# Kernel optimization log

Measured on AMD Instinct MI355X. Metric: run time of the kernel, lower is better.

## Reference

```python
import jax, jax.numpy as jnp
import numpy as np

B, T, D, O = 16, 1024, 1024, 10  # broadcast in original requires T == D

def setup_inputs() -> dict:
    key = jax.random.key(0)
    k1, k2, k3 = jax.random.split(key, 3)
    logits = jax.random.normal(k1, (B, T, D), dtype=jnp.float32)
    decision = jax.random.uniform(k2, (B, T, O), dtype=jnp.float32)  # unused by forward math
    W = jax.random.normal(k3, (O, D), dtype=jnp.float32) * 0.02  # attention.weight
    b = jnp.zeros((O,), dtype=jnp.float32)                       # attention.bias
    return {"logits": logits, "decision": decision, "W": W, "b": b}

def reference(logits, decision, W, b):
    outputdim = W.shape[0]
    # w_x = softmax(Linear(logits)/outputdim, dim=1)  -> softmax over time T
    scores = (jnp.einsum('btd,od->bto', logits, W) + b) / outputdim  # (B,T,O)
    w_x = jax.nn.softmax(scores, axis=1)
    # Original materializes h[b,i,o,t] = logits[b,t,i] * w_x[b,i,o] (needs T==D),
    # then flattens (o,t) and sums over dim 1 (i). Equivalent contraction:
    # out[b,o,t] = sum_i logits[b,t,i] * w_x[b,i,o]
    out = jnp.einsum('bti,bio->bot', logits, w_x)  # (B,O,T)
    return out.reshape(logits.shape[0], -1)        # (B, O*T)
```

## Files before the change

kernel.cpp:

```cpp
#include <hip/hip_runtime.h>

#define BB 16
#define TT 1024
#define DD 1024
#define OO 10

template <bool BIAS>
__global__ __launch_bounds__(256) void gemm10_kernel(
    const float* __restrict__ X,
    const float* __restrict__ Wt,
    const float* __restrict__ bias,
    float* __restrict__ Y,
    float scale, int perBatchW)
{
    __shared__ float sW[OO * DD];
    __shared__ float part[4][32][OO];

    const int b   = blockIdx.y;
    const int t0  = blockIdx.x * 32;
    const int tid = threadIdx.x;

    {
        const float4* src = (const float4*)(Wt + (size_t)(perBatchW ? b : 0) * (OO * DD));
        float4* dst = (float4*)sW;
#pragma unroll
        for (int c = 0; c < 10; ++c)
            dst[c * 256 + tid] = src[c * 256 + tid];
    }
    __syncthreads();

    const int w    = tid >> 6;
    const int lane = tid & 63;
    const int l    = lane & 7;
    const int g    = lane >> 3;
    const int dofs = w * 256 + l * 4;

    const float* xp[4];
#pragma unroll
    for (int j = 0; j < 4; ++j)
        xp[j] = X + ((size_t)b * TT + t0 + g + 8 * j) * DD + dofs;
    const float* sWl = sW + dofs;

    float acc[4][OO];
#pragma unroll
    for (int j = 0; j < 4; ++j)
#pragma unroll
        for (int o = 0; o < OO; ++o) acc[j][o] = 0.f;

    float4 x0[4], x1[4];
#pragma unroll
    for (int j = 0; j < 4; ++j) {
        x0[j] = *(const float4*)(xp[j]);
        x1[j] = *(const float4*)(xp[j] + 32);
    }

#pragma unroll 1
    for (int it = 0; it < 8; it += 2) {
        float4 c0[4];
#pragma unroll
        for (int j = 0; j < 4; ++j) c0[j] = x0[j];
        if (it < 6) {
#pragma unroll
            for (int j = 0; j < 4; ++j)
                x0[j] = *(const float4*)(xp[j] + (it + 2) * 32);
        }
        {
            const float* wp = sWl + it * 32;
#pragma unroll
            for (int o = 0; o < OO; ++o) {
                const float4 wv = *(const float4*)(wp + o * DD);
#pragma unroll
                for (int j = 0; j < 4; ++j)
                    acc[j][o] += c0[j].x * wv.x + c0[j].y * wv.y +
                                 c0[j].z * wv.z + c0[j].w * wv.w;
            }
        }
#pragma unroll
        for (int j = 0; j < 4; ++j) c0[j] = x1[j];
        if (it < 5) {
#pragma unroll
            for (int j = 0; j < 4; ++j)
                x1[j] = *(const float4*)(xp[j] + (it + 3) * 32);
        }
        {
            const float* wp = sWl + (it + 1) * 32;
#pragma unroll
            for (int o = 0; o < OO; ++o) {
                const float4 wv = *(const float4*)(wp + o * DD);
#pragma unroll
                for (int j = 0; j < 4; ++j)
                    acc[j][o] += c0[j].x * wv.x + c0[j].y * wv.y +
                                 c0[j].z * wv.z + c0[j].w * wv.w;
            }
        }
    }

#pragma unroll
    for (int j = 0; j < 4; ++j) {
#pragma unroll
        for (int o = 0; o < OO; ++o) {
            float v = acc[j][o];
            v += __shfl_down(v, 4, 8);
            v += __shfl_down(v, 2, 8);
            v += __shfl_down(v, 1, 8);
            if (l == 0) part[w][j * 8 + g][o] = v;
        }
    }
    __syncthreads();

    for (int idx = tid; idx < 32 * OO; idx += 256) {
        const int row = idx / OO;
        const int o   = idx % OO;
        float v = part[0][row][o] + part[1][row][o] +
                  part[2][row][o] + part[3][row][o];
        if (BIAS) v = (v + bias[o]) * scale;
        Y[((size_t)b * OO + o) * TT + (t0 + row)] = v;
    }
}

__global__ __launch_bounds__(256) void softmax_kernel(float* __restrict__ s)
{
    float* col = s + (size_t)blockIdx.x * TT;
    const int tid  = threadIdx.x;
    const int wave = tid >> 6;
    const int lane = tid & 63;

    float4 v = *(const float4*)(col + tid * 4);

    __shared__ float sm[4];
    __shared__ float ss[4];

    float m = fmaxf(fmaxf(v.x, v.y), fmaxf(v.z, v.w));
#pragma unroll
    for (int off = 32; off > 0; off >>= 1) m = fmaxf(m, __shfl_down(m, off, 64));
    if (lane == 0) sm[wave] = m;
    __syncthreads();
    m = fmaxf(fmaxf(sm[0], sm[1]), fmaxf(sm[2], sm[3]));

    float e0 = __expf(v.x - m), e1 = __expf(v.y - m);
    float e2 = __expf(v.z - m), e3 = __expf(v.w - m);
    float sum = e0 + e1 + e2 + e3;
#pragma unroll
    for (int off = 32; off > 0; off >>= 1) sum += __shfl_down(sum, off, 64);
    if (lane == 0) ss[wave] = sum;
    __syncthreads();
    const float inv = 1.0f / (ss[0] + ss[1] + ss[2] + ss[3]);

    *(float4*)(col + tid * 4) = make_float4(e0 * inv, e1 * inv, e2 * inv, e3 * inv);
}

extern "C" void kernel_launch(void* const* d_in, const int* in_sizes, int n_in,
                              void* d_out, int out_size, void* d_ws, size_t ws_size,
                              hipStream_t stream)
{
    const float* logits = (const float*)d_in[0];
    const float* W    = (const float*)d_in[2];
    const float* bias = (const float*)d_in[3];
    float* out    = (float*)d_out;
    float* scores = (float*)d_ws;

    dim3 grid(TT / 32, BB);
    gemm10_kernel<true><<<grid, 256, 0, stream>>>(logits, W, bias, scores,
                                                  1.0f / OO, 0);
    softmax_kernel<<<BB * OO, 256, 0, stream>>>(scores);
    gemm10_kernel<false><<<grid, 256, 0, stream>>>(logits, scores, nullptr, out,
                                                   1.0f, 1);
}
```

Baseline: 120.7 us.

## Stage X tiles through padded double-buffered shared memory for coalesced loads

```diff
diff --git a/kernel.cpp b/kernel.cpp
--- a/kernel.cpp
+++ b/kernel.cpp
@@ -13,8 +13,9 @@
     float* __restrict__ Y,
     float scale, int perBatchW)
 {
-    __shared__ float sW[OO * DD];
-    __shared__ float part[4][32][OO];
+    __shared__ float4 sW4[OO * 256];
+    __shared__ float4 sX[2][32 * 33];
+    __shared__ float  part[4][32][OO];
 
     const int b   = blockIdx.y;
     const int t0  = blockIdx.x * 32;
@@ -22,10 +23,23 @@
 
     {
         const float4* src = (const float4*)(Wt + (size_t)(perBatchW ? b : 0) * (OO * DD));
-        float4* dst = (float4*)sW;
 #pragma unroll
         for (int c = 0; c < 10; ++c)
-            dst[c * 256 + tid] = src[c * 256 + tid];
+            sW4[c * 256 + tid] = src[c * 256 + tid];
+    }
+
+    const int srow = tid >> 5;
+    const int scol = tid & 31;
+    const float4* Xb = (const float4*)(X + ((size_t)b * TT + t0) * DD);
+
+    {
+        float4 st[4];
+#pragma unroll
+        for (int k = 0; k < 4; ++k)
+            st[k] = Xb[(size_t)(srow + 8 * k) * 256 + scol];
+#pragma unroll
+        for (int k = 0; k < 4; ++k)
+            sX[0][(srow + 8 * k) * 33 + scol] = st[k];
     }
     __syncthreads();
 
@@ -33,13 +47,7 @@
     const int lane = tid & 63;
     const int l    = lane & 7;
     const int g    = lane >> 3;
-    const int dofs = w * 256 + l * 4;
-
-    const float* xp[4];
-#pragma unroll
-    for (int j = 0; j < 4; ++j)
-        xp[j] = X + ((size_t)b * TT + t0 + g + 8 * j) * DD + dofs;
-    const float* sWl = sW + dofs;
+    const int xoff = w * 8 + l;
 
     float acc[4][OO];
 #pragma unroll
@@ -47,52 +55,35 @@
 #pragma unroll
         for (int o = 0; o < OO; ++o) acc[j][o] = 0.f;
 
-    float4 x0[4], x1[4];
+#pragma unroll 1
+    for (int c = 0; c < 8; ++c) {
+        float4 st[4];
+        if (c < 7) {
 #pragma unroll
-    for (int j = 0; j < 4; ++j) {
-        x0[j] = *(const float4*)(xp[j]);
-        x1[j] = *(const float4*)(xp[j] + 32);
-    }
+            for (int k = 0; k < 4; ++k)
+                st[k] = Xb[(size_t)(srow + 8 * k) * 256 + (c + 1) * 32 + scol];
+        }
 
-#pragma unroll 1
-    for (int it = 0; it < 8; it += 2) {
-        float4 c0[4];
+        const float4* xb = sX[c & 1];
+        float4 xf[4];
 #pragma unroll
-        for (int j = 0; j < 4; ++j) c0[j] = x0[j];
-        if (it < 6) {
+        for (int j = 0; j < 4; ++j)
+            xf[j] = xb[(g + 8 * j) * 33 + xoff];
+#pragma unroll
+        for (int o = 0; o < OO; ++o) {
+            const float4 wv = sW4[o * 256 + c * 32 + xoff];
 #pragma unroll
             for (int j = 0; j < 4; ++j)
-                x0[j] = *(const float4*)(xp[j] + (it + 2) * 32);
+                acc[j][o] += xf[j].x * wv.x + xf[j].y * wv.y +
+                             xf[j].z * wv.z + xf[j].w * wv.w;
         }
-        {
-            const float* wp = sWl + it * 32;
+
+        if (c < 7) {
 #pragma unroll
-            for (int o = 0; o < OO; ++o) {
-                const float4 wv = *(const float4*)(wp + o * DD);
-#pragma unroll
-                for (int j = 0; j < 4; ++j)
-                    acc[j][o] += c0[j].x * wv.x + c0[j].y * wv.y +
-                                 c0[j].z * wv.z + c0[j].w * wv.w;
-            }
+            for (int k = 0; k < 4; ++k)
+                sX[(c + 1) & 1][(srow + 8 * k) * 33 + scol] = st[k];
         }
-#pragma unroll
-        for (int j = 0; j < 4; ++j) c0[j] = x1[j];
-        if (it < 5) {
-#pragma unroll
-            for (int j = 0; j < 4; ++j)
-                x1[j] = *(const float4*)(xp[j] + (it + 3) * 32);
-        }
-        {
-            const float* wp = sWl + (it + 1) * 32;
-#pragma unroll
-            for (int o = 0; o < OO; ++o) {
-                const float4 wv = *(const float4*)(wp + o * DD);
-#pragma unroll
-                for (int j = 0; j < 4; ++j)
-                    acc[j][o] += c0[j].x * wv.x + c0[j].y * wv.y +
-                                 c0[j].z * wv.z + c0[j].w * wv.w;
-            }
-        }
+        __syncthreads();
     }
 
 #pragma unroll
```

Result: slower. 144.4 us (+19.6%).

## Fuse score GEMM, softmax, and pooling GEMM into one kernel with per-batch barrier

Applied to the files above, without the earlier changes.

```diff
diff --git a/kernel.cpp b/kernel.cpp
--- a/kernel.cpp
+++ b/kernel.cpp
@@ -5,27 +5,27 @@
 #define DD 1024
 #define OO 10
 
-template <bool BIAS>
-__global__ __launch_bounds__(256) void gemm10_kernel(
+__global__ __launch_bounds__(256, 2) void fused_attnpool_kernel(
     const float* __restrict__ X,
     const float* __restrict__ Wt,
     const float* __restrict__ bias,
-    float* __restrict__ Y,
-    float scale, int perBatchW)
+    float* __restrict__ out,
+    float* __restrict__ scores,
+    unsigned int* __restrict__ ctr)
 {
-    __shared__ float sW[OO * DD];
-    __shared__ float part[4][32][OO];
+    __shared__ float4 sW4[OO * 256];
+    __shared__ float  part[4][32][OO];
+    __shared__ float  red[4][OO];
 
     const int b   = blockIdx.y;
     const int t0  = blockIdx.x * 32;
     const int tid = threadIdx.x;
 
     {
-        const float4* src = (const float4*)(Wt + (size_t)(perBatchW ? b : 0) * (OO * DD));
-        float4* dst = (float4*)sW;
+        const float4* src = (const float4*)Wt;
 #pragma unroll
         for (int c = 0; c < 10; ++c)
-            dst[c * 256 + tid] = src[c * 256 + tid];
+            sW4[c * 256 + tid] = src[c * 256 + tid];
     }
     __syncthreads();
 
@@ -39,72 +39,71 @@
 #pragma unroll
     for (int j = 0; j < 4; ++j)
         xp[j] = X + ((size_t)b * TT + t0 + g + 8 * j) * DD + dofs;
-    const float* sWl = sW + dofs;
-
-    float acc[4][OO];
-#pragma unroll
-    for (int j = 0; j < 4; ++j)
-#pragma unroll
-        for (int o = 0; o < OO; ++o) acc[j][o] = 0.f;
-
-    float4 x0[4], x1[4];
-#pragma unroll
-    for (int j = 0; j < 4; ++j) {
-        x0[j] = *(const float4*)(xp[j]);
-        x1[j] = *(const float4*)(xp[j] + 32);
-    }
+    const float* sWl = (const float*)sW4 + dofs;
+
+    {
+        float acc[4][OO];
+#pragma unroll
+        for (int j = 0; j < 4; ++j)
+#pragma unroll
+            for (int o = 0; o < OO; ++o) acc[j][o] = 0.f;
+
+        float4 x0[4], x1[4];
+#pragma unroll
+        for (int j = 0; j < 4; ++j) {
+            x0[j] = *(const float4*)(xp[j]);
+            x1[j] = *(const float4*)(xp[j] + 32);
+        }
 
 #pragma unroll 1
-    for (int it = 0; it < 8; it += 2) {
-        float4 c0[4];
-#pragma unroll
-        for (int j = 0; j < 4; ++j) c0[j] = x0[j];
-        if (it < 6) {
-#pragma unroll
-            for (int j = 0; j < 4; ++j)
-                x0[j] = *(const float4*)(xp[j] + (it + 2) * 32);
-        }
-        {
-            const float* wp = sWl + it * 32;
+        for (int it = 0; it < 8; it += 2) {
+            float4 c0[4];
+#pragma unroll
+            for (int j = 0; j < 4; ++j) c0[j] = x0[j];
+            if (it < 6)
+#pragma unroll
+                for (int j = 0; j < 4; ++j)
+                    x0[j] = *(const float4*)(xp[j] + (it + 2) * 32);
+            {
+                const float* wp = sWl + it * 32;
+#pragma unroll
+                for (int o = 0; o < OO; ++o) {
+                    const float4 wv = *(const float4*)(wp + o * DD);
+#pragma unroll
+                    for (int j = 0; j < 4; ++j)
+                        acc[j][o] += c0[j].x * wv.x + c0[j].y * wv.y +
+                                     c0[j].z * wv.z + c0[j].w * wv.w;
+                }
+            }
+#pragma unroll
+            for (int j = 0; j < 4; ++j) c0[j] = x1[j];
+            if (it < 5)
+#pragma unroll
+                for (int j = 0; j < 4; ++j)
+                    x1[j] = *(const float4*)(xp[j] + (it + 3) * 32);
+            {
+                const float* wp = sWl + (it + 1) * 32;
+#pragma unroll
+                for (int o = 0; o < OO; ++o) {
+                    const float4 wv = *(const float4*)(wp + o * DD);
+#pragma unroll
+                    for (int j = 0; j < 4; ++j)
+                        acc[j][o] += c0[j].x * wv.x + c0[j].y * wv.y +
+                                     c0[j].z * wv.z + c0[j].w * wv.w;
+                }
+            }
+        }
+
+#pragma unroll
+        for (int j = 0; j < 4; ++j)
 #pragma unroll
             for (int o = 0; o < OO; ++o) {
-                const float4 wv = *(const float4*)(wp + o * DD);
-#pragma unroll
-                for (int j = 0; j < 4; ++j)
-                    acc[j][o] += c0[j].x * wv.x + c0[j].y * wv.y +
-                                 c0[j].z * wv.z + c0[j].w * wv.w;
-            }
-        }
-#pragma unroll
-        for (int j = 0; j < 4; ++j) c0[j] = x1[j];
-        if (it < 5) {
-#pragma unroll
-            for (int j = 0; j < 4; ++j)
-                x1[j] = *(const float4*)(xp[j] + (it + 3) * 32);
-        }
-        {
-            const float* wp = sWl + (it + 1) * 32;
-#pragma unroll
-            for (int o = 0; o < OO; ++o) {
-                const float4 wv = *(const float4*)(wp + o * DD);
-#pragma unroll
-                for (int j = 0; j < 4; ++j)
-                    acc[j][o] += c0[j].x * wv.x + c0[j].y * wv.y +
-                                 c0[j].z * wv.z + c0[j].w * wv.w;
-            }
-        }
-    }
-
-#pragma unroll
-    for (int j = 0; j < 4; ++j) {
-#pragma unroll
-        for (int o = 0; o < OO; ++o) {
-            float v = acc[j][o];
-            v += __shfl_down(v, 4, 8);
-            v += __shfl_down(v, 2, 8);
-            v += __shfl_down(v, 1, 8);
-            if (l == 0) part[w][j * 8 + g][o] = v;
-        }
+                float v = acc[j][o];
+                v += __shfl_down(v, 4, 8);
+                v += __shfl_down(v, 2, 8);
+                v += __shfl_down(v, 1, 8);
+                if (l == 0) part[w][j * 8 + g][o] = v;
+            }
     }
     __syncthreads();
 
@@ -113,40 +112,151 @@
         const int o   = idx % OO;
         float v = part[0][row][o] + part[1][row][o] +
                   part[2][row][o] + part[3][row][o];
-        if (BIAS) v = (v + bias[o]) * scale;
-        Y[((size_t)b * OO + o) * TT + (t0 + row)] = v;
-    }
-}
-
-__global__ __launch_bounds__(256) void softmax_kernel(float* __restrict__ s)
-{
-    float* col = s + (size_t)blockIdx.x * TT;
-    const int tid  = threadIdx.x;
-    const int wave = tid >> 6;
-    const int lane = tid & 63;
-
-    float4 v = *(const float4*)(col + tid * 4);
-
-    __shared__ float sm[4];
-    __shared__ float ss[4];
-
-    float m = fmaxf(fmaxf(v.x, v.y), fmaxf(v.z, v.w));
-#pragma unroll
-    for (int off = 32; off > 0; off >>= 1) m = fmaxf(m, __shfl_down(m, off, 64));
-    if (lane == 0) sm[wave] = m;
-    __syncthreads();
-    m = fmaxf(fmaxf(sm[0], sm[1]), fmaxf(sm[2], sm[3]));
-
-    float e0 = __expf(v.x - m), e1 = __expf(v.y - m);
-    float e2 = __expf(v.z - m), e3 = __expf(v.w - m);
-    float sum = e0 + e1 + e2 + e3;
-#pragma unroll
-    for (int off = 32; off > 0; off >>= 1) sum += __shfl_down(sum, off, 64);
-    if (lane == 0) ss[wave] = sum;
-    __syncthreads();
-    const float inv = 1.0f / (ss[0] + ss[1] + ss[2] + ss[3]);
-
-    *(float4*)(col + tid * 4) = make_float4(e0 * inv, e1 * inv, e2 * inv, e3 * inv);
+        v = (v + bias[o]) * (1.0f / OO);
+        __hip_atomic_store(&scores[((size_t)b * OO + o) * TT + (t0 + row)], v,
+                           __ATOMIC_RELAXED, __HIP_MEMORY_SCOPE_AGENT);
+    }
+    __syncthreads();
+
+    if (tid == 0) {
+        __threadfence();
+        atomicAdd(&ctr[b], 1u);
+        while (__hip_atomic_load(&ctr[b], __ATOMIC_RELAXED,
+                                 __HIP_MEMORY_SCOPE_AGENT) < 32u)
+            __builtin_amdgcn_s_sleep(8);
+    }
+    __syncthreads();
+    __threadfence();
+
+    {
+        float4 sv[OO];
+        float  mo[OO];
+        const float* sb = scores + (size_t)b * OO * TT;
+#pragma unroll
+        for (int o = 0; o < OO; ++o) {
+            const float* p = sb + (size_t)o * TT + tid * 4;
+            float4 v = make_float4(p[0], p[1], p[2], p[3]);
+            sv[o] = v;
+            mo[o] = fmaxf(fmaxf(v.x, v.y), fmaxf(v.z, v.w));
+        }
+#pragma unroll
+        for (int o = 0; o < OO; ++o) {
+            float m = mo[o];
+#pragma unroll
+            for (int off = 32; off > 0; off >>= 1)
+                m = fmaxf(m, __shfl_down(m, off, 64));
+            if (lane == 0) red[w][o] = m;
+        }
+        __syncthreads();
+        float M[OO];
+#pragma unroll
+        for (int o = 0; o < OO; ++o)
+            M[o] = fmaxf(fmaxf(red[0][o], red[1][o]),
+                         fmaxf(red[2][o], red[3][o]));
+        __syncthreads();
+
+        float so[OO];
+#pragma unroll
+        for (int o = 0; o < OO; ++o) {
+            float4 v = sv[o];
+            v.x = __expf(v.x - M[o]); v.y = __expf(v.y - M[o]);
+            v.z = __expf(v.z - M[o]); v.w = __expf(v.w - M[o]);
+            sv[o] = v;
+            so[o] = v.x + v.y + v.z + v.w;
+        }
+#pragma unroll
+        for (int o = 0; o < OO; ++o) {
+            float s = so[o];
+#pragma unroll
+            for (int off = 32; off > 0; off >>= 1)
+                s += __shfl_down(s, off, 64);
+            if (lane == 0) red[w][o] = s;
+        }
+        __syncthreads();
+#pragma unroll
+        for (int o = 0; o < OO; ++o) {
+            const float inv = 1.0f / (red[0][o] + red[1][o] +
+                                      red[2][o] + red[3][o]);
+            float4 v = sv[o];
+            sW4[o * 256 + tid] =
+                make_float4(v.x * inv, v.y * inv, v.z * inv, v.w * inv);
+        }
+    }
+    __syncthreads();
+
+    {
+        float acc[4][OO];
+#pragma unroll
+        for (int j = 0; j < 4; ++j)
+#pragma unroll
+            for (int o = 0; o < OO; ++o) acc[j][o] = 0.f;
+
+        float4 x0[4], x1[4];
+#pragma unroll
+        for (int j = 0; j < 4; ++j) {
+            x0[j] = *(const float4*)(xp[j]);
+            x1[j] = *(const float4*)(xp[j] + 32);
+        }
+
+#pragma unroll 1
+        for (int it = 0; it < 8; it += 2) {
+            float4 c0[4];
+#pragma unroll
+            for (int j = 0; j < 4; ++j) c0[j] = x0[j];
+            if (it < 6)
+#pragma unroll
+                for (int j = 0; j < 4; ++j)
+                    x0[j] = *(const float4*)(xp[j] + (it + 2) * 32);
+            {
+                const float* wp = sWl + it * 32;
+#pragma unroll
+                for (int o = 0; o < OO; ++o) {
+                    const float4 wv = *(const float4*)(wp + o * DD);
+#pragma unroll
+                    for (int j = 0; j < 4; ++j)
+                        acc[j][o] += c0[j].x * wv.x + c0[j].y * wv.y +
+                                     c0[j].z * wv.z + c0[j].w * wv.w;
+                }
+            }
+#pragma unroll
+            for (int j = 0; j < 4; ++j) c0[j] = x1[j];
+            if (it < 5)
+#pragma unroll
+                for (int j = 0; j < 4; ++j)
+                    x1[j] = *(const float4*)(xp[j] + (it + 3) * 32);
+            {
+                const float* wp = sWl + (it + 1) * 32;
+#pragma unroll
+                for (int o = 0; o < OO; ++o) {
+                    const float4 wv = *(const float4*)(wp + o * DD);
+#pragma unroll
+                    for (int j = 0; j < 4; ++j)
+                        acc[j][o] += c0[j].x * wv.x + c0[j].y * wv.y +
+                                     c0[j].z * wv.z + c0[j].w * wv.w;
+                }
+            }
+        }
+
+#pragma unroll
+        for (int j = 0; j < 4; ++j)
+#pragma unroll
+            for (int o = 0; o < OO; ++o) {
+                float v = acc[j][o];
+                v += __shfl_down(v, 4, 8);
+                v += __shfl_down(v, 2, 8);
+                v += __shfl_down(v, 1, 8);
+                if (l == 0) part[w][j * 8 + g][o] = v;
+            }
+    }
+    __syncthreads();
+
+    for (int idx = tid; idx < 32 * OO; idx += 256) {
+        const int row = idx / OO;
+        const int o   = idx % OO;
+        out[((size_t)b * OO + o) * TT + (t0 + row)] =
+            part[0][row][o] + part[1][row][o] +
+            part[2][row][o] + part[3][row][o];
+    }
 }
 
 extern "C" void kernel_launch(void* const* d_in, const int* in_sizes, int n_in,
@@ -157,12 +267,13 @@
     const float* W    = (const float*)d_in[2];
     const float* bias = (const float*)d_in[3];
     float* out    = (float*)d_out;
-    float* scores = (float*)d_ws;
+
+    float*        scores = (float*)d_ws;
+    unsigned int* ctr    = (unsigned int*)((char*)d_ws + (4 << 20));
+
+    (void)hipMemsetAsync(ctr, 0, BB * sizeof(unsigned int), stream);
 
     dim3 grid(TT / 32, BB);
-    gemm10_kernel<true><<<grid, 256, 0, stream>>>(logits, W, bias, scores,
-                                                  1.0f / OO, 0);
-    softmax_kernel<<<BB * OO, 256, 0, stream>>>(scores);
-    gemm10_kernel<false><<<grid, 256, 0, stream>>>(logits, scores, nullptr, out,
-                                                   1.0f, 1);
+    fused_attnpool_kernel<<<grid, 256, 0, stream>>>(logits, W, bias, out,
+                                                    scores, ctr);
 }
```

After: 193.9 us. 60.6% more time.

## Fuse softmax into score GEMM epilogue with atomic normalizer and deferred division

Applied to the files above, without the earlier changes.

```diff
diff --git a/kernel.cpp b/kernel.cpp
--- a/kernel.cpp
+++ b/kernel.cpp
@@ -5,27 +5,27 @@
 #define DD 1024
 #define OO 10
 
-template <bool BIAS>
+template <bool FIRST>
 __global__ __launch_bounds__(256) void gemm10_kernel(
     const float* __restrict__ X,
     const float* __restrict__ Wt,
     const float* __restrict__ bias,
     float* __restrict__ Y,
-    float scale, int perBatchW)
+    float* __restrict__ Z)
 {
-    __shared__ float sW[OO * DD];
-    __shared__ float part[4][32][OO];
+    __shared__ float4 sW4[OO * 256];
+    __shared__ float  part[4][32][OO];
+    __shared__ float  uv[32][OO];
 
     const int b   = blockIdx.y;
     const int t0  = blockIdx.x * 32;
     const int tid = threadIdx.x;
 
     {
-        const float4* src = (const float4*)(Wt + (size_t)(perBatchW ? b : 0) * (OO * DD));
-        float4* dst = (float4*)sW;
+        const float4* src = (const float4*)(Wt + (FIRST ? 0 : (size_t)b * OO * TT));
 #pragma unroll
         for (int c = 0; c < 10; ++c)
-            dst[c * 256 + tid] = src[c * 256 + tid];
+            sW4[c * 256 + tid] = src[c * 256 + tid];
     }
     __syncthreads();
 
@@ -39,7 +39,7 @@
 #pragma unroll
     for (int j = 0; j < 4; ++j)
         xp[j] = X + ((size_t)b * TT + t0 + g + 8 * j) * DD + dofs;
-    const float* sWl = sW + dofs;
+    const float* sWl = (const float*)sW4 + dofs;
 
     float acc[4][OO];
 #pragma unroll
@@ -113,40 +113,25 @@
         const int o   = idx % OO;
         float v = part[0][row][o] + part[1][row][o] +
                   part[2][row][o] + part[3][row][o];
-        if (BIAS) v = (v + bias[o]) * scale;
-        Y[((size_t)b * OO + o) * TT + (t0 + row)] = v;
+        if (FIRST) {
+            float u = __expf((v + bias[o]) * (1.0f / OO));
+            Y[((size_t)b * OO + o) * TT + (t0 + row)] = u;
+            uv[row][o] = u;
+        } else {
+            const float invZ = 1.0f / Z[b * OO + o];
+            Y[((size_t)b * OO + o) * TT + (t0 + row)] = v * invZ;
+        }
     }
-}
 
-__global__ __launch_bounds__(256) void softmax_kernel(float* __restrict__ s)
-{
-    float* col = s + (size_t)blockIdx.x * TT;
-    const int tid  = threadIdx.x;
-    const int wave = tid >> 6;
-    const int lane = tid & 63;
-
-    float4 v = *(const float4*)(col + tid * 4);
-
-    __shared__ float sm[4];
-    __shared__ float ss[4];
-
-    float m = fmaxf(fmaxf(v.x, v.y), fmaxf(v.z, v.w));
+    if (FIRST) {
+        __syncthreads();
+        if (tid < OO) {
+            float s = 0.f;
 #pragma unroll
-    for (int off = 32; off > 0; off >>= 1) m = fmaxf(m, __shfl_down(m, off, 64));
-    if (lane == 0) sm[wave] = m;
-    __syncthreads();
-    m = fmaxf(fmaxf(sm[0], sm[1]), fmaxf(sm[2], sm[3]));
-
-    float e0 = __expf(v.x - m), e1 = __expf(v.y - m);
-    float e2 = __expf(v.z - m), e3 = __expf(v.w - m);
-    float sum = e0 + e1 + e2 + e3;
-#pragma unroll
-    for (int off = 32; off > 0; off >>= 1) sum += __shfl_down(sum, off, 64);
-    if (lane == 0) ss[wave] = sum;
-    __syncthreads();
-    const float inv = 1.0f / (ss[0] + ss[1] + ss[2] + ss[3]);
-
-    *(float4*)(col + tid * 4) = make_float4(e0 * inv, e1 * inv, e2 * inv, e3 * inv);
+            for (int row = 0; row < 32; ++row) s += uv[row][tid];
+            atomicAdd(&Z[b * OO + tid], s);
+        }
+    }
 }
 
 extern "C" void kernel_launch(void* const* d_in, const int* in_sizes, int n_in,
@@ -156,13 +141,14 @@
     const float* logits = (const float*)d_in[0];
     const float* W    = (const float*)d_in[2];
     const float* bias = (const float*)d_in[3];
-    float* out    = (float*)d_out;
-    float* scores = (float*)d_ws;
+    float* out = (float*)d_out;
+
+    float* u = (float*)d_ws;
+    float* Z = (float*)((char*)d_ws + (4 << 20));
+
+    (void)hipMemsetAsync(Z, 0, BB * OO * sizeof(float), stream);
 
     dim3 grid(TT / 32, BB);
-    gemm10_kernel<true><<<grid, 256, 0, stream>>>(logits, W, bias, scores,
-                                                  1.0f / OO, 0);
-    softmax_kernel<<<BB * OO, 256, 0, stream>>>(scores);
-    gemm10_kernel<false><<<grid, 256, 0, stream>>>(logits, scores, nullptr, out,
-                                                   1.0f, 1);
+    gemm10_kernel<true><<<grid, 256, 0, stream>>>(logits, W, bias, u, Z);
+    gemm10_kernel<false><<<grid, 256, 0, stream>>>(logits, u, nullptr, out, Z);
 }
```

Result: no change. 120.3 us (-0.4%).
